# Performance work log

Measured on AMD Instinct MI355X. Metric: run time of the kernel, lower is better.

Reference implementation:

```python
import jax, jax.numpy as jnp
import numpy as np

NEG_SLOPE = 0.2  # PyG GATv2 default negative_slope
EPS = 1e-16      # PyG softmax denominator epsilon


def gatv2_conv(x, edge_index, Wl, Wr, att, bias):
    """GATv2Conv, concat=True, add_self_loops=False, share_weights=False.
    x: [N, F]; edge_index: [2, E] (row0=src j, row1=dst i);
    Wl, Wr: [F, H*C]; att: [H, C]; bias: [H*C]. Returns [N, H*C]."""
    N = x.shape[0]
    H, C = att.shape
    src, dst = edge_index[0], edge_index[1]
    xl = (x @ Wl).reshape(N, H, C)  # source-side transform
    xr = (x @ Wr).reshape(N, H, C)  # target-side transform
    # per-edge attention logits: a . leaky_relu(xl_j + xr_i)  -> [E, H]
    e = jnp.einsum('ehc,hc->eh', jax.nn.leaky_relu(xl[src] + xr[dst], NEG_SLOPE), att)
    # segment softmax over incoming edges of each dst node
    emax = jax.ops.segment_max(e, dst, num_segments=N)          # [N, H]
    ex = jnp.exp(e - emax[dst])                                  # [E, H]
    denom = jax.ops.segment_sum(ex, dst, num_segments=N)        # [N, H]
    alpha = ex / (denom[dst] + EPS)                              # [E, H]
    out = jax.ops.segment_sum(alpha[:, :, None] * xl[src], dst, num_segments=N)  # [N, H, C]
    return out.reshape(N, H * C) + bias


def setup_inputs() -> dict:
    key = jax.random.key(0)
    ks = jax.random.split(key, 16)
    N, F, E, H, C = 50000, 128, 500000, 4, 32
    HC = H * C  # 128; layer2 input dim = HC
    OUT = 4
    s_in = 1.0 / np.sqrt(F)
    s_h = 1.0 / np.sqrt(HC)
    inp = {
        'x': jax.random.normal(ks[0], (N, F), jnp.float32),
        'edge_for': jax.random.randint(ks[1], (2, E), 0, N, jnp.int32),
        'edge_against': jax.random.randint(ks[2], (2, E), 0, N, jnp.int32),
        'edge_vote': jax.random.randint(ks[3], (2, E), 0, N, jnp.int32),
        # layer 1 params, stacked over the 3 relations
        'W1l': jax.random.normal(ks[4], (3, F, HC), jnp.float32) * s_in,
        'W1r': jax.random.normal(ks[5], (3, F, HC), jnp.float32) * s_in,
        'att1': jax.random.normal(ks[6], (3, H, C), jnp.float32) * (1.0 / np.sqrt(C)),
        'b1': jnp.zeros((3, HC), jnp.float32),
        # layer 2 params
        'W2l': jax.random.normal(ks[7], (3, HC, HC), jnp.float32) * s_h,
        'W2r': jax.random.normal(ks[8], (3, HC, HC), jnp.float32) * s_h,
        'att2': jax.random.normal(ks[9], (3, H, C), jnp.float32) * (1.0 / np.sqrt(C)),
        'b2': jnp.zeros((3, HC), jnp.float32),
        # final classifier: in = HC*4 (4 players grouped per game)
        'fcW': jax.random.normal(ks[10], (HC * 4, OUT), jnp.float32) * (1.0 / np.sqrt(HC * 4)),
        'fcb': jnp.zeros((OUT,), jnp.float32),
    }
    return inp


def reference(x, edge_for, edge_against, edge_vote,
              W1l, W1r, att1, b1, W2l, W2r, att2, b2, fcW, fcb):
    edges = [edge_for, edge_against, edge_vote]

    def hetero(xin, Wl, Wr, att, b):
        out = gatv2_conv(xin, edges[0], Wl[0], Wr[0], att[0], b[0])
        for r in (1, 2):  # HeteroConv aggr='sum' over relations
            out = out + gatv2_conv(xin, edges[r], Wl[r], Wr[r], att[r], b[r])
        return out

    h = hetero(x, W1l, W1r, att1, b1)        # [N, H*C]
    h = hetero(h, W2l, W2r, att2, b2)        # [N, H*C]
    h = h.reshape(-1, h.shape[1] * 4)        # [N/4, H*C*4]
    h = jax.nn.relu(h)                       # dropout is identity in eval
    return h @ fcW + fcb                     # [N/4, 4]
```

## Files before the change

kernel.cpp:

```cpp
#include <hip/hip_runtime.h>
#include <hip/hip_bf16.h>
#include <math.h>

#define NEG_SLOPE 0.2f
#define SM_EPS 1e-16f
#define SCAN_CHUNK 4096

typedef short bf16x8 __attribute__((ext_vector_type(8)));
typedef float f32x16 __attribute__((ext_vector_type(16)));
typedef unsigned short ushort8 __attribute__((ext_vector_type(8)));
typedef unsigned short ushort4v __attribute__((ext_vector_type(4)));

__device__ inline unsigned short f2bf(float f) {
    unsigned int u = __float_as_uint(f);
    unsigned int r = (u + 0x7FFF + ((u >> 16) & 1)) >> 16;
    return (unsigned short)r;
}


__global__ void count_deg3(const int* __restrict__ e0, const int* __restrict__ e1,
                           const int* __restrict__ e2, int* __restrict__ deg3,
                           int E, int N) {
    int r = blockIdx.y;
    const int* edge = (r == 0) ? e0 : (r == 1) ? e1 : e2;
    int t = blockIdx.x * blockDim.x + threadIdx.x;
    if (t < E) atomicAdd(&deg3[(size_t)r * N + edge[E + t]], 1);
}

__global__ __launch_bounds__(256) void scan_partial(const int* __restrict__ deg3,
                                                    int* __restrict__ bsum,
                                                    int N, int nblk) {
    int r = blockIdx.y;
    const int* deg = deg3 + (size_t)r * N;
    int tid = threadIdx.x;
    int tbase = blockIdx.x * SCAN_CHUNK + tid * 16;
    int sum = 0;
    #pragma unroll
    for (int k = 0; k < 16; ++k) {
        int i = tbase + k;
        if (i < N) sum += deg[i];
    }
    #pragma unroll
    for (int off = 1; off < 64; off <<= 1) sum += __shfl_xor(sum, off);
    __shared__ int ws[4];
    int lane = tid & 63, wid = tid >> 6;
    if (lane == 0) ws[wid] = sum;
    __syncthreads();
    if (tid == 0) bsum[(size_t)r * nblk + blockIdx.x] = ws[0] + ws[1] + ws[2] + ws[3];
}

__global__ void scan_mid(int* __restrict__ bsum, int* __restrict__ rp3,
                         int N, int nblk) {
    int r = blockIdx.x;
    int* bs = bsum + (size_t)r * nblk;
    int tid = threadIdx.x;
    int v = (tid < nblk) ? bs[tid] : 0;
    int lane = tid & 63, wid = tid >> 6;
    int incl = v;
    #pragma unroll
    for (int off = 1; off < 64; off <<= 1) {
        int t2 = __shfl_up(incl, off);
        if (lane >= off) incl += t2;
    }
    __shared__ int ws[4];
    if (lane == 63) ws[wid] = incl;
    __syncthreads();
    int woff = 0;
    #pragma unroll
    for (int q = 0; q < 4; ++q) woff += (q < wid) ? ws[q] : 0;
    if (tid < nblk) bs[tid] = woff + incl - v;
    if (tid == 255) rp3[(size_t)r * (N + 1) + N] = woff + incl;
}

__global__ __launch_bounds__(256) void scan_apply(const int* __restrict__ deg3,
                                                  const int* __restrict__ bsum,
                                                  int* __restrict__ rp3,
                                                  int* __restrict__ cur3,
                                                  int N, int nblk) {
    int r = blockIdx.y;
    const int* deg = deg3 + (size_t)r * N;
    int* rp  = rp3 + (size_t)r * (N + 1);
    int* cur = cur3 + (size_t)r * N;
    int boff = bsum[(size_t)r * nblk + blockIdx.x];
    int tid = threadIdx.x;
    int tbase = blockIdx.x * SCAN_CHUNK + tid * 16;
    int vals[16];
    int s = 0;
    #pragma unroll
    for (int k = 0; k < 16; ++k) {
        int i = tbase + k;
        vals[k] = (i < N) ? deg[i] : 0;
        s += vals[k];
    }
    int lane = tid & 63, wid = tid >> 6;
    int incl = s;
    #pragma unroll
    for (int off = 1; off < 64; off <<= 1) {
        int t2 = __shfl_up(incl, off);
        if (lane >= off) incl += t2;
    }
    __shared__ int ws[4];
    if (lane == 63) ws[wid] = incl;
    __syncthreads();
    int woff = 0;
    #pragma unroll
    for (int q = 0; q < 4; ++q) woff += (q < wid) ? ws[q] : 0;
    int run = boff + woff + (incl - s);
    #pragma unroll
    for (int k = 0; k < 16; ++k) {
        int i = tbase + k;
        if (i < N) { rp[i] = run; cur[i] = run; }
        run += vals[k];
    }
}

__global__ void scatter3(const int* __restrict__ e0, const int* __restrict__ e1,
                         const int* __restrict__ e2, int* __restrict__ cur3,
                         int* __restrict__ csrc3, int E, int N) {
    int r = blockIdx.y;
    const int* edge = (r == 0) ? e0 : (r == 1) ? e1 : e2;
    int t = blockIdx.x * blockDim.x + threadIdx.x;
    if (t < E) {
        int src = edge[t];
        int dst = edge[E + t];
        int pos = atomicAdd(&cur3[(size_t)r * N + dst], 1);
        csrc3[(size_t)r * E + pos] = src;
    }
}


__global__ void cast_bf16(const float* __restrict__ in, unsigned short* __restrict__ out,
                          int n4) {
    int t = blockIdx.x * blockDim.x + threadIdx.x;
    if (t < n4) {
        float4 v = *(const float4*)(in + (size_t)t * 4);
        ushort4v o = {f2bf(v.x), f2bf(v.y), f2bf(v.z), f2bf(v.w)};
        *(ushort4v*)(out + (size_t)t * 4) = o;
    }
}

__global__ __launch_bounds__(256) void transpose_cast_w(
    const float* __restrict__ W1l, const float* __restrict__ W1r,
    const float* __restrict__ W2l, const float* __restrict__ W2r,
    unsigned short* __restrict__ WT) {
    const float* srcs[4] = {W1l, W1r, W2l, W2r};
    int g = blockIdx.z, r = blockIdx.y;
    const float* W = srcs[g] + (size_t)r * 16384;
    unsigned short* D = WT + (size_t)(g * 3 + r) * 16384;
    int t = blockIdx.x;
    int kr = (t >> 2) * 32, cb = (t & 3) * 32;
    __shared__ float tile[32][33];
    int tr = threadIdx.x >> 3, tc4 = (threadIdx.x & 7) * 4;
    float4 v = *(const float4*)(W + (size_t)(kr + tr) * 128 + cb + tc4);
    tile[tr][tc4 + 0] = v.x;
    tile[tr][tc4 + 1] = v.y;
    tile[tr][tc4 + 2] = v.z;
    tile[tr][tc4 + 3] = v.w;
    __syncthreads();
    int c = threadIdx.x >> 3, k4 = (threadIdx.x & 7) * 4;
    ushort4v o = {f2bf(tile[k4 + 0][c]), f2bf(tile[k4 + 1][c]),
                  f2bf(tile[k4 + 2][c]), f2bf(tile[k4 + 3][c])};
    *(ushort4v*)(D + (size_t)(cb + c) * 128 + kr + k4) = o;
}


__global__ __launch_bounds__(256) void gemm_mfma(
    const unsigned short* __restrict__ Abf,
    const unsigned short* __restrict__ WTl,
    const unsigned short* __restrict__ WTr,
    unsigned short* __restrict__ C0, unsigned short* __restrict__ C1, int M) {
    __shared__ unsigned short As[128][136];
    __shared__ unsigned short Bs[64][136];
    int tid = threadIdx.x;
    int bm = blockIdx.x * 128;
    int y = blockIdx.y;
    const unsigned short* WT = (y < 2 ? WTl : WTr) + (size_t)(y & 1) * 64 * 128;
    unsigned short* C = (y < 2) ? C0 : C1;
    int bcol = (y & 1) * 64;

    #pragma unroll
    for (int i = 0; i < 8; ++i) {
        int c = tid + i * 256;
        int row = c >> 4, ko = (c & 15) * 8;
        int gr = bm + row; if (gr >= M) gr = M - 1;
        ushort8 v = *(const ushort8*)(Abf + (size_t)gr * 128 + ko);
        *(ushort8*)(&As[row][ko]) = v;
    }
    #pragma unroll
    for (int i = 0; i < 4; ++i) {
        int c = tid + i * 256;
        int row = c >> 4, ko = (c & 15) * 8;
        ushort8 v = *(const ushort8*)(WT + (size_t)row * 128 + ko);
        *(ushort8*)(&Bs[row][ko]) = v;
    }
    __syncthreads();

    int wid = tid >> 6, lane = tid & 63;
    int wr = (wid >> 1) * 64, wc = (wid & 1) * 32;
    int la = lane & 31, lb = (lane >> 5) * 8;
    f32x16 acc0 = {};
    f32x16 acc1 = {};
    #pragma unroll
    for (int ks = 0; ks < 8; ++ks) {
        int k0 = ks * 16;
        bf16x8 a0 = *(const bf16x8*)(&As[wr + la][k0 + lb]);
        bf16x8 a1 = *(const bf16x8*)(&As[wr + 32 + la][k0 + lb]);
        bf16x8 b  = *(const bf16x8*)(&Bs[wc + la][k0 + lb]);
        acc0 = __builtin_amdgcn_mfma_f32_32x32x16_bf16(a0, b, acc0, 0, 0, 0);
        acc1 = __builtin_amdgcn_mfma_f32_32x32x16_bf16(a1, b, acc1, 0, 0, 0);
    }

    int col = bcol + wc + la;
    int rbase = (lane >> 5) * 4;
    #pragma unroll
    for (int reg = 0; reg < 16; ++reg) {
        int rr = (reg & 3) + 8 * (reg >> 2) + rbase;
        int row0 = bm + wr + rr;
        if (row0 < M) C[(size_t)row0 * 128 + col] = f2bf(acc0[reg]);
        int row1 = bm + wr + 32 + rr;
        if (row1 < M) C[(size_t)row1 * 128 + col] = f2bf(acc1[reg]);
    }
}


__global__ __launch_bounds__(256) void edge_fused(const unsigned int* __restrict__ XL2,
                                                  const unsigned int* __restrict__ XR2,
                                                  const int* __restrict__ rp,
                                                  const int* __restrict__ csrc,
                                                  const float* __restrict__ att,
                                                  float* __restrict__ hout, int N) {
    int lane = threadIdx.x & 63;
    int node = blockIdx.x * 4 + (threadIdx.x >> 6);
    if (node >= N) return;
    int c0 = lane * 2;
    float2 a2 = *(const float2*)(att + c0);
    unsigned int xru = XR2[(size_t)node * 64 + lane];
    float xrx = __uint_as_float(xru << 16);
    float xry = __uint_as_float(xru & 0xFFFF0000u);
    int s = rp[node], e = rp[node + 1];
    float m = -INFINITY, den = 0.f, ax = 0.f, ay = 0.f;

#define EF_LOGIT(u, tx, xx, yy)                                       \
    {                                                                 \
        xx = __uint_as_float((u) << 16);                              \
        yy = __uint_as_float((u) & 0xFFFF0000u);                      \
        float v0 = xx + xrx; v0 = (v0 > 0.f) ? v0 : NEG_SLOPE * v0;   \
        float v1 = yy + xry; v1 = (v1 > 0.f) ? v1 : NEG_SLOPE * v1;   \
        tx = fmaf(v0, a2.x, v1 * a2.y);                               \
    }
#define EF_UPDATE(tx, xx, yy)                                         \
    {                                                                 \
        float mnew = fmaxf(m, tx);                                    \
        float sc = __expf(m - mnew);                                  \
        float p = __expf(tx - mnew);                                  \
        den = fmaf(den, sc, p);                                       \
        ax  = fmaf(ax, sc, p * xx);                                   \
        ay  = fmaf(ay, sc, p * yy);                                   \
        m = mnew;                                                     \
    }

    int j = s;
    for (; j + 8 <= e; j += 8) {
        int s0 = csrc[j],     s1 = csrc[j + 1], s2 = csrc[j + 2], s3 = csrc[j + 3];
        int s4 = csrc[j + 4], s5 = csrc[j + 5], s6 = csrc[j + 6], s7 = csrc[j + 7];
        unsigned int u0 = XL2[(size_t)s0 * 64 + lane];
        unsigned int u1 = XL2[(size_t)s1 * 64 + lane];
        unsigned int u2 = XL2[(size_t)s2 * 64 + lane];
        unsigned int u3 = XL2[(size_t)s3 * 64 + lane];
        unsigned int u4 = XL2[(size_t)s4 * 64 + lane];
        unsigned int u5 = XL2[(size_t)s5 * 64 + lane];
        unsigned int u6 = XL2[(size_t)s6 * 64 + lane];
        unsigned int u7 = XL2[(size_t)s7 * 64 + lane];
        float t0, t1, t2, t3, t4, t5, t6, t7;
        float x0, x1, x2, x3, x4, x5, x6, x7;
        float y0, y1, y2, y3, y4, y5, y6, y7;
        EF_LOGIT(u0, t0, x0, y0);
        EF_LOGIT(u1, t1, x1, y1);
        EF_LOGIT(u2, t2, x2, y2);
        EF_LOGIT(u3, t3, x3, y3);
        EF_LOGIT(u4, t4, x4, y4);
        EF_LOGIT(u5, t5, x5, y5);
        EF_LOGIT(u6, t6, x6, y6);
        EF_LOGIT(u7, t7, x7, y7);
        #pragma unroll
        for (int off = 1; off < 16; off <<= 1) {
            t0 += __shfl_xor(t0, off);
            t1 += __shfl_xor(t1, off);
            t2 += __shfl_xor(t2, off);
            t3 += __shfl_xor(t3, off);
            t4 += __shfl_xor(t4, off);
            t5 += __shfl_xor(t5, off);
            t6 += __shfl_xor(t6, off);
            t7 += __shfl_xor(t7, off);
        }
        EF_UPDATE(t0, x0, y0);
        EF_UPDATE(t1, x1, y1);
        EF_UPDATE(t2, x2, y2);
        EF_UPDATE(t3, x3, y3);
        EF_UPDATE(t4, x4, y4);
        EF_UPDATE(t5, x5, y5);
        EF_UPDATE(t6, x6, y6);
        EF_UPDATE(t7, x7, y7);
    }
    for (; j + 4 <= e; j += 4) {
        int s0 = csrc[j], s1 = csrc[j + 1], s2 = csrc[j + 2], s3 = csrc[j + 3];
        unsigned int u0 = XL2[(size_t)s0 * 64 + lane];
        unsigned int u1 = XL2[(size_t)s1 * 64 + lane];
        unsigned int u2 = XL2[(size_t)s2 * 64 + lane];
        unsigned int u3 = XL2[(size_t)s3 * 64 + lane];
        float t0, t1, t2, t3, x0, x1, x2, x3, y0, y1, y2, y3;
        EF_LOGIT(u0, t0, x0, y0);
        EF_LOGIT(u1, t1, x1, y1);
        EF_LOGIT(u2, t2, x2, y2);
        EF_LOGIT(u3, t3, x3, y3);
        #pragma unroll
        for (int off = 1; off < 16; off <<= 1) {
            t0 += __shfl_xor(t0, off);
            t1 += __shfl_xor(t1, off);
            t2 += __shfl_xor(t2, off);
            t3 += __shfl_xor(t3, off);
        }
        EF_UPDATE(t0, x0, y0);
        EF_UPDATE(t1, x1, y1);
        EF_UPDATE(t2, x2, y2);
        EF_UPDATE(t3, x3, y3);
    }
    for (; j < e; ++j) {
        int src = csrc[j];
        unsigned int u0 = XL2[(size_t)src * 64 + lane];
        float t0, x0, y0;
        EF_LOGIT(u0, t0, x0, y0);
        #pragma unroll
        for (int off = 1; off < 16; off <<= 1) t0 += __shfl_xor(t0, off);
        EF_UPDATE(t0, x0, y0);
    }
#undef EF_LOGIT
#undef EF_UPDATE

    float inv = 1.f / (den + SM_EPS);
    float2* hp = (float2*)(hout + (size_t)node * 128 + c0);
    float2 o = *hp;
    o.x = fmaf(ax, inv, o.x);
    o.y = fmaf(ay, inv, o.y);
    *hp = o;
}

__global__ void init_h(float* __restrict__ h, const float* __restrict__ b3, int total4) {
    int t = blockIdx.x * blockDim.x + threadIdx.x;
    if (t < total4) {
        int c = (t & 31) * 4;
        float4 b0 = *(const float4*)(b3 + c);
        float4 b1 = *(const float4*)(b3 + 128 + c);
        float4 b2 = *(const float4*)(b3 + 256 + c);
        float4 o = {b0.x + b1.x + b2.x, b0.y + b1.y + b2.y,
                    b0.z + b1.z + b2.z, b0.w + b1.w + b2.w};
        *(float4*)(h + (size_t)t * 4) = o;
    }
}

__global__ __launch_bounds__(256) void final_fc(const float* __restrict__ h2,
                                                const float* __restrict__ fcW,
                                                const float* __restrict__ fcb,
                                                float* __restrict__ out, int G) {
    int lane = threadIdx.x & 63;
    int g = blockIdx.x * 4 + (threadIdx.x >> 6);
    if (g >= G) return;
    const float* hv = h2 + (size_t)g * 512 + lane * 8;
    float4 p0 = *(const float4*)hv;
    float4 p1 = *(const float4*)(hv + 4);
    float v[8] = {p0.x, p0.y, p0.z, p0.w, p1.x, p1.y, p1.z, p1.w};
    float acc0 = 0, acc1 = 0, acc2 = 0, acc3 = 0;
    #pragma unroll
    for (int jj = 0; jj < 8; ++jj) {
        float xv = v[jj] > 0.f ? v[jj] : 0.f;
        float4 w = *(const float4*)(fcW + (size_t)(lane * 8 + jj) * 4);
        acc0 = fmaf(xv, w.x, acc0);
        acc1 = fmaf(xv, w.y, acc1);
        acc2 = fmaf(xv, w.z, acc2);
        acc3 = fmaf(xv, w.w, acc3);
    }
    #pragma unroll
    for (int off = 1; off < 64; off <<= 1) {
        acc0 += __shfl_xor(acc0, off);
        acc1 += __shfl_xor(acc1, off);
        acc2 += __shfl_xor(acc2, off);
        acc3 += __shfl_xor(acc3, off);
    }
    if (lane == 0) {
        float4 o = {acc0 + fcb[0], acc1 + fcb[1], acc2 + fcb[2], acc3 + fcb[3]};
        *(float4*)(out + (size_t)g * 4) = o;
    }
}


extern "C" void kernel_launch(void* const* d_in, const int* in_sizes, int n_in,
                              void* d_out, int out_size, void* d_ws, size_t ws_size,
                              hipStream_t stream) {
    const float* x    = (const float*)d_in[0];
    const int*   e_f  = (const int*)d_in[1];
    const int*   e_a  = (const int*)d_in[2];
    const int*   e_v  = (const int*)d_in[3];
    const float* W1l  = (const float*)d_in[4];
    const float* W1r  = (const float*)d_in[5];
    const float* att1 = (const float*)d_in[6];
    const float* b1   = (const float*)d_in[7];
    const float* W2l  = (const float*)d_in[8];
    const float* W2r  = (const float*)d_in[9];
    const float* att2 = (const float*)d_in[10];
    const float* b2   = (const float*)d_in[11];
    const float* fcW  = (const float*)d_in[12];
    const float* fcb  = (const float*)d_in[13];
    float* out = (float*)d_out;

    int N = in_sizes[0] / 128;
    int E = in_sizes[1] / 2;
    int nblk = (N + SCAN_CHUNK - 1) / SCAN_CHUNK;

    char* ws = (char*)d_ws;
    size_t off = 0;
    auto alloc = [&](size_t bytes) -> void* {
        void* p = ws + off;
        off += (bytes + 255) & ~size_t(255);
        return p;
    };
    int*   deg3  = (int*)alloc((size_t)3 * N * 4);
    int*   cur3  = (int*)alloc((size_t)3 * N * 4);
    int*   rp3   = (int*)alloc((size_t)3 * (N + 1) * 4);
    int*   csrc3 = (int*)alloc((size_t)3 * E * 4);
    int*   bsum  = (int*)alloc((size_t)3 * 256 * 4);
    unsigned short* XLbf = (unsigned short*)alloc((size_t)N * 128 * 2);
    unsigned short* XRbf = (unsigned short*)alloc((size_t)N * 128 * 2);
    float* h1    = (float*)alloc((size_t)N * 128 * 4);
    float* h2    = (float*)alloc((size_t)N * 128 * 4);
    unsigned short* Abf = (unsigned short*)alloc((size_t)N * 128 * 2);
    unsigned short* WT  = (unsigned short*)alloc((size_t)12 * 128 * 128 * 2);

    hipMemsetAsync(deg3, 0, (size_t)3 * N * 4, stream);
    int ecb = (E + 255) / 256;
    count_deg3<<<dim3(ecb, 3), 256, 0, stream>>>(e_f, e_a, e_v, deg3, E, N);
    scan_partial<<<dim3(nblk, 3), 256, 0, stream>>>(deg3, bsum, N, nblk);
    scan_mid<<<3, 256, 0, stream>>>(bsum, rp3, N, nblk);
    scan_apply<<<dim3(nblk, 3), 256, 0, stream>>>(deg3, bsum, rp3, cur3, N, nblk);
    scatter3<<<dim3(ecb, 3), 256, 0, stream>>>(e_f, e_a, e_v, cur3, csrc3, E, N);

    transpose_cast_w<<<dim3(16, 3, 4), 256, 0, stream>>>(W1l, W1r, W2l, W2r, WT);

    int nb_rows  = (N + 127) / 128;
    int nb_node4 = (N + 3) / 4;
    int nb_init  = (N * 128 / 4 + 255) / 256;
    int nb_cast  = (N * 128 / 4 + 255) / 256;

    struct Layer {
        const float *in, *att, *b;
        int wtg_l, wtg_r;
        float* hout;
    };
    Layer layers[2] = {
        { x,  att1, b1, 0, 1, h1 },
        { h1, att2, b2, 2, 3, h2 },
    };

    for (int L = 0; L < 2; ++L) {
        Layer& ly = layers[L];
        cast_bf16<<<nb_cast, 256, 0, stream>>>(ly.in, Abf, N * 128 / 4);
        init_h<<<nb_init, 256, 0, stream>>>(ly.hout, ly.b, N * 128 / 4);
        for (int r = 0; r < 3; ++r) {
            const unsigned short* WTl = WT + (size_t)(ly.wtg_l * 3 + r) * 16384;
            const unsigned short* WTr = WT + (size_t)(ly.wtg_r * 3 + r) * 16384;
            gemm_mfma<<<dim3(nb_rows, 4), 256, 0, stream>>>(Abf, WTl, WTr, XLbf, XRbf, N);
            const int* rp   = rp3 + (size_t)r * (N + 1);
            const int* csrc = csrc3 + (size_t)r * E;
            edge_fused<<<nb_node4, 256, 0, stream>>>((const unsigned int*)XLbf,
                                                     (const unsigned int*)XRbf, rp, csrc,
                                                     ly.att + (size_t)r * 128, ly.hout, N);
        }
    }
    int G = N / 4;
    final_fc<<<(G + 3) / 4, 256, 0, stream>>>(h2, fcW, fcb, out, G);
}
```

Measured before the change: 640.4 us.

## Replace direct CSR scatter with two-pass bucketed binning by destination range

The single-pass atomic scatter of edges into CSR order is replaced by a two-stage radix-like pass. Edges are first binned by destination blocks of 1024 nodes through shared-memory staging and coalesced writes. A second kernel then scatters each bin locally, so the per-node atomics and csrc writes hit a small, cache-resident range. This adds an extra kernel launch pair, an 8-byte-per-edge intermediate buffer and extra memory traffic in exchange for better locality. It relies on N fitting in 64 bins of 1024, i.e. N <= 65536.

Result: faster. 611.7 us (-4.5%).

```diff
diff --git a/kernel.cpp b/kernel.cpp
--- a/kernel.cpp
+++ b/kernel.cpp
@@ -5,6 +5,7 @@
 #define NEG_SLOPE 0.2f
 #define SM_EPS 1e-16f
 #define SCAN_CHUNK 4096
+#define BIN_SHIFT 10
 
 typedef short bf16x8 __attribute__((ext_vector_type(8)));
 typedef float f32x16 __attribute__((ext_vector_type(16)));
@@ -114,17 +115,92 @@
     }
 }
 
-__global__ void scatter3(const int* __restrict__ e0, const int* __restrict__ e1,
-                         const int* __restrict__ e2, int* __restrict__ cur3,
-                         int* __restrict__ csrc3, int E, int N) {
+__global__ void init_gcur(const int* __restrict__ rp3, int* __restrict__ gcur, int N) {
+    int r = blockIdx.x, b = threadIdx.x;
+    int idx = b << BIN_SHIFT;
+    if (idx > N) idx = N;
+    gcur[r * 64 + b] = rp3[(size_t)r * (N + 1) + idx];
+}
+
+__global__ __launch_bounds__(256) void bin_edges(const int* __restrict__ e0,
+                                                 const int* __restrict__ e1,
+                                                 const int* __restrict__ e2,
+                                                 int* __restrict__ gcur,
+                                                 uint2* __restrict__ ebin,
+                                                 int E, int N) {
     int r = blockIdx.y;
     const int* edge = (r == 0) ? e0 : (r == 1) ? e1 : e2;
-    int t = blockIdx.x * blockDim.x + threadIdx.x;
-    if (t < E) {
-        int src = edge[t];
-        int dst = edge[E + t];
-        int pos = atomicAdd(&cur3[(size_t)r * N + dst], 1);
-        csrc3[(size_t)r * E + pos] = src;
+    __shared__ uint2 stage[4096];
+    __shared__ unsigned char sbin[4096];
+    __shared__ int cnt[64], curb[64], offc[64], gbase[64];
+    int tid = threadIdx.x;
+    if (tid < 64) cnt[tid] = 0;
+    __syncthreads();
+    int base = blockIdx.x * 4096;
+    int mysrc[16], mydst[16];
+    #pragma unroll
+    for (int k = 0; k < 16; ++k) {
+        int i = base + k * 256 + tid;
+        int sv = -1, dv = 0;
+        if (i < E) {
+            sv = edge[i];
+            dv = edge[E + i];
+            atomicAdd(&cnt[dv >> BIN_SHIFT], 1);
+        }
+        mysrc[k] = sv; mydst[k] = dv;
+    }
+    __syncthreads();
+    if (tid < 64) {
+        int c = cnt[tid];
+        int incl = c;
+        #pragma unroll
+        for (int off = 1; off < 64; off <<= 1) {
+            int t2 = __shfl_up(incl, off);
+            if (tid >= off) incl += t2;
+        }
+        int excl = incl - c;
+        offc[tid] = excl;
+        curb[tid] = excl;
+        gbase[tid] = (c > 0) ? atomicAdd(&gcur[r * 64 + tid], c) : 0;
+    }
+    __syncthreads();
+    #pragma unroll
+    for (int k = 0; k < 16; ++k) {
+        if (mysrc[k] >= 0) {
+            int b = mydst[k] >> BIN_SHIFT;
+            int p = atomicAdd(&curb[b], 1);
+            stage[p] = make_uint2((unsigned)mysrc[k], (unsigned)mydst[k]);
+            sbin[p] = (unsigned char)b;
+        }
+    }
+    __syncthreads();
+    int total = offc[63] + cnt[63];
+    for (int s = tid; s < total; s += 256) {
+        int b = sbin[s];
+        ebin[(size_t)r * E + gbase[b] + (s - offc[b])] = stage[s];
+    }
+}
+
+__global__ __launch_bounds__(256) void scatter_local(const uint2* __restrict__ ebin,
+                                                     const int* __restrict__ rp3,
+                                                     int* __restrict__ cur3,
+                                                     int* __restrict__ csrc3,
+                                                     int E, int N) {
+    int r = blockIdx.z, b = blockIdx.y, z = blockIdx.x;
+    int nb1 = b << BIN_SHIFT;
+    if (nb1 >= N) return;
+    int nb2 = (b + 1) << BIN_SHIFT;
+    if (nb2 > N) nb2 = N;
+    const int* rp = rp3 + (size_t)r * (N + 1);
+    int s0 = rp[nb1], s1 = rp[nb2];
+    int len = s1 - s0;
+    int per = (len + (int)gridDim.x - 1) / (int)gridDim.x;
+    int a0 = s0 + z * per;
+    int a1 = a0 + per; if (a1 > s1) a1 = s1;
+    for (int i = a0 + threadIdx.x; i < a1; i += 256) {
+        uint2 ed = ebin[(size_t)r * E + i];
+        int pos = atomicAdd(&cur3[(size_t)r * N + (int)ed.y], 1);
+        csrc3[(size_t)r * E + pos] = (int)ed.x;
     }
 }
 
@@ -428,6 +504,8 @@
     int*   rp3   = (int*)alloc((size_t)3 * (N + 1) * 4);
     int*   csrc3 = (int*)alloc((size_t)3 * E * 4);
     int*   bsum  = (int*)alloc((size_t)3 * 256 * 4);
+    int*   gcur  = (int*)alloc((size_t)3 * 64 * 4);
+    uint2* ebin  = (uint2*)alloc((size_t)3 * E * 8);
     unsigned short* XLbf = (unsigned short*)alloc((size_t)N * 128 * 2);
     unsigned short* XRbf = (unsigned short*)alloc((size_t)N * 128 * 2);
     float* h1    = (float*)alloc((size_t)N * 128 * 4);
@@ -437,11 +515,14 @@
 
     hipMemsetAsync(deg3, 0, (size_t)3 * N * 4, stream);
     int ecb = (E + 255) / 256;
+    int ebb = (E + 4095) / 4096;
     count_deg3<<<dim3(ecb, 3), 256, 0, stream>>>(e_f, e_a, e_v, deg3, E, N);
     scan_partial<<<dim3(nblk, 3), 256, 0, stream>>>(deg3, bsum, N, nblk);
     scan_mid<<<3, 256, 0, stream>>>(bsum, rp3, N, nblk);
     scan_apply<<<dim3(nblk, 3), 256, 0, stream>>>(deg3, bsum, rp3, cur3, N, nblk);
-    scatter3<<<dim3(ecb, 3), 256, 0, stream>>>(e_f, e_a, e_v, cur3, csrc3, E, N);
+    init_gcur<<<3, 64, 0, stream>>>(rp3, gcur, N);
+    bin_edges<<<dim3(ebb, 3), 256, 0, stream>>>(e_f, e_a, e_v, gcur, ebin, E, N);
+    scatter_local<<<dim3(8, 64, 3), 256, 0, stream>>>(ebin, rp3, cur3, csrc3, E, N);
 
     transpose_cast_w<<<dim3(16, 3, 4), 256, 0, stream>>>(W1l, W1r, W2l, W2r, WT);
 
```
